# Optimization experiments

Measured on AMD Instinct MI355X. Metric: run time of the kernel, lower is better.

The kernel has to match this reference:

```python
import jax, jax.numpy as jnp
import numpy as np

N, NFEAT = 8192, 128

def _unif(k, shape, fan_out):
    s = 1.0 / np.sqrt(fan_out)
    return jax.random.uniform(k, shape, jnp.float32, -s, s)

def setup_inputs() -> dict:
    key = jax.random.key(0)
    ks = jax.random.split(key, 10)
    x = jax.random.normal(ks[0], (N, NFEAT), jnp.float32)
    adj = jax.random.uniform(ks[1], (N, N), jnp.float32)  # all > 0 -> full degree
    W1 = _unif(ks[2], (NFEAT, 10), 10); b1 = _unif(ks[3], (10,), 10)
    W2 = _unif(ks[4], (10, 5), 5);      b2 = _unif(ks[5], (5,), 5)
    fc1_W = _unif(ks[6], (5, 5), 5);    fc1_b = _unif(ks[7], (5,), 5)
    fc_W = _unif(ks[8], (5, 2), 2);     fc_b = _unif(ks[9], (2,), 2)
    return dict(x=x, adj=adj, W1=W1, b1=b1, W2=W2, b2=b2,
                fc1_W=fc1_W, fc1_b=fc1_b, fc_W=fc_W, fc_b=fc_b)

def _gcn(x, adj, W, b):
    # D = diag(row-wise count of adj > 0); A_tilda = D^-1/2 (A + I) D^-1/2
    deg = jnp.sum((adj > 0.0).astype(x.dtype), axis=1)
    dinv = deg ** -0.5                       # [N]
    s = (x @ W) * dinv[:, None]              # D^-1/2 @ (X W), [N, out]
    out = dinv[:, None] * (adj @ s + s)      # D^-1/2 @ (A + I) @ s
    return out + b

def reference(x, adj, W1, b1, W2, b2, fc1_W, fc1_b, fc_W, fc_b):
    h = jax.nn.relu(_gcn(x, adj, W1, b1))    # [N, 10]
    h = _gcn(h, adj, W2, b2)                 # [N, 5]
    z = jax.nn.relu(jnp.mean(h, axis=0))     # [5]
    z2 = jax.nn.relu(z @ fc1_W + fc1_b)      # [5]
    y = jax.nn.sigmoid(z2 @ fc_W + fc_b)     # [2]
    return (z, y)
```

## Files before the change

kernel.cpp:

```cpp
#include <hip/hip_runtime.h>
#include <math.h>

#define NN 8192
#define NF 128


__global__ __launch_bounds__(256) void kS1p(const float* __restrict__ x,
                                            const float* __restrict__ W1,
                                            float* __restrict__ s1p) {
    __shared__ float sW[NF * 10];
    for (int i = threadIdx.x; i < NF * 10; i += 256) sW[i] = W1[i];
    __syncthreads();
    int tid = blockIdx.x * 256 + threadIdx.x;
    int j = tid / 10, k = tid % 10;
    const float4* xr = (const float4*)(x + (size_t)j * NF);
    float s = 0.f;
#pragma unroll
    for (int f4 = 0; f4 < 32; f4++) {
        float4 a = xr[f4];
        s += a.x * sW[(f4 * 4 + 0) * 10 + k] + a.y * sW[(f4 * 4 + 1) * 10 + k]
           + a.z * sW[(f4 * 4 + 2) * 10 + k] + a.w * sW[(f4 * 4 + 3) * 10 + k];
    }
    s1p[tid] = s;
}

__global__ __launch_bounds__(512) void kFuse(const float* __restrict__ adj,
                                             const float* __restrict__ s1p,
                                             float* __restrict__ accO,
                                             float* __restrict__ dinv,
                                             float* __restrict__ c0,
                                             int* __restrict__ Zcount,
                                             int* __restrict__ Zlist) {
    __shared__ float lcs[4][2048];
    const int t = threadIdx.x;
    const int lane = t & 63, wid = t >> 6;
    for (int n = t; n < 8192; n += 512) ((float*)lcs)[n] = 0.f;
    __syncthreads();

    const int i0 = blockIdx.x * 32 + wid * 4;
    float acc[4][10];
#pragma unroll
    for (int r = 0; r < 4; r++)
#pragma unroll
        for (int k = 0; k < 10; k++) acc[r][k] = 0.f;
    int cnt[4] = {0, 0, 0, 0};

    const float4* a0p = (const float4*)(adj + (size_t)(i0 + 0) * NN);
    const float4* a1p = (const float4*)(adj + (size_t)(i0 + 1) * NN);
    const float4* a2p = (const float4*)(adj + (size_t)(i0 + 2) * NN);
    const float4* a3p = (const float4*)(adj + (size_t)(i0 + 3) * NN);

    for (int it = 0; it < 32; it++) {
        const int vi = it * 64 + lane;
        float4 a0 = a0p[vi], a1 = a1p[vi], a2 = a2p[vi], a3 = a3p[vi];
        const float4* sp = (const float4*)(s1p + (size_t)vi * 40);
        float sv[40];
#pragma unroll
        for (int q = 0; q < 10; q++) {
            float4 v = sp[q];
            sv[q * 4 + 0] = v.x; sv[q * 4 + 1] = v.y;
            sv[q * 4 + 2] = v.z; sv[q * 4 + 3] = v.w;
        }
#pragma unroll
        for (int k = 0; k < 10; k++) {
            acc[0][k] += a0.x * sv[k] + a0.y * sv[10 + k] + a0.z * sv[20 + k] + a0.w * sv[30 + k];
            acc[1][k] += a1.x * sv[k] + a1.y * sv[10 + k] + a1.z * sv[20 + k] + a1.w * sv[30 + k];
            acc[2][k] += a2.x * sv[k] + a2.y * sv[10 + k] + a2.z * sv[20 + k] + a2.w * sv[30 + k];
            acc[3][k] += a3.x * sv[k] + a3.y * sv[10 + k] + a3.z * sv[20 + k] + a3.w * sv[30 + k];
        }
        atomicAdd(&lcs[0][vi], a0.x + a1.x + a2.x + a3.x);
        atomicAdd(&lcs[1][vi], a0.y + a1.y + a2.y + a3.y);
        atomicAdd(&lcs[2][vi], a0.z + a1.z + a2.z + a3.z);
        atomicAdd(&lcs[3][vi], a0.w + a1.w + a2.w + a3.w);
        cnt[0] += (a0.x > 0.f) + (a0.y > 0.f) + (a0.z > 0.f) + (a0.w > 0.f);
        cnt[1] += (a1.x > 0.f) + (a1.y > 0.f) + (a1.z > 0.f) + (a1.w > 0.f);
        cnt[2] += (a2.x > 0.f) + (a2.y > 0.f) + (a2.z > 0.f) + (a2.w > 0.f);
        cnt[3] += (a3.x > 0.f) + (a3.y > 0.f) + (a3.z > 0.f) + (a3.w > 0.f);
    }

#pragma unroll
    for (int r = 0; r < 4; r++) {
#pragma unroll
        for (int k = 0; k < 10; k++)
#pragma unroll
            for (int off = 32; off > 0; off >>= 1)
                acc[r][k] += __shfl_xor(acc[r][k], off, 64);
#pragma unroll
        for (int off = 32; off > 0; off >>= 1)
            cnt[r] += __shfl_xor(cnt[r], off, 64);
    }

    if (lane == 0) {
#pragma unroll
        for (int r = 0; r < 4; r++) {
            const int i = i0 + r;
            dinv[i] = rsqrtf((float)cnt[r]);
            if (cnt[r] != NN) { int p = atomicAdd(Zcount, 1); Zlist[p] = i; }
#pragma unroll
            for (int k = 0; k < 10; k++) accO[i * 10 + k] = acc[r][k];
        }
    }

    __syncthreads();
    for (int n = t; n < 8192; n += 512)
        atomicAdd(&c0[n], lcs[n & 3][n >> 2]);
}

__global__ __launch_bounds__(256) void kTail(const float* __restrict__ adj,
                                             const float* __restrict__ accI,
                                             const float* __restrict__ s1p,
                                             const float* __restrict__ dinv,
                                             const float* __restrict__ c0,
                                             const int* __restrict__ Zcount,
                                             const int* __restrict__ Zlist,
                                             const float* __restrict__ b1,
                                             const float* __restrict__ W2,
                                             float* __restrict__ accum) {
    const int j = blockIdx.x * 256 + threadIdx.x;
    const float dinv0 = rsqrtf((float)NN);
    const float dj = dinv[j];
    float cj = c0[j] * dinv0;
    float hv[10];
#pragma unroll
    for (int k = 0; k < 10; k++) hv[k] = dinv0 * accI[j * 10 + k];

    const int zc = *Zcount;
    for (int p = 0; p < zc; p++) {
        const int zi = Zlist[p];
        const float dz = dinv[zi] - dinv0;
        cj += dz * adj[(size_t)zi * NN + j];
        const float az = dz * adj[(size_t)j * NN + zi];
#pragma unroll
        for (int k = 0; k < 10; k++) hv[k] += az * s1p[zi * 10 + k];
    }
#pragma unroll
    for (int k = 0; k < 10; k++)
        hv[k] = fmaxf(dj * (hv[k] + dj * s1p[j * 10 + k]) + b1[k], 0.f);

    float p10[10];
#pragma unroll
    for (int k = 0; k < 5; k++) {
        float s = 0.f;
#pragma unroll
        for (int m = 0; m < 10; m++) s += hv[m] * W2[m * 5 + k];
        s *= dj;
        p10[k] = cj * s;
        p10[5 + k] = dj * s;
    }
#pragma unroll
    for (int q = 0; q < 10; q++) {
        float v = p10[q];
#pragma unroll
        for (int off = 32; off > 0; off >>= 1) v += __shfl_xor(v, off, 64);
        if ((threadIdx.x & 63) == 0) atomicAdd(&accum[q], v);
    }
}

__global__ void kF2(const float* __restrict__ accum, const float* __restrict__ b2,
                    const float* __restrict__ fc1W, const float* __restrict__ fc1b,
                    const float* __restrict__ fcW, const float* __restrict__ fcb,
                    float* __restrict__ out) {
    if (threadIdx.x == 0 && blockIdx.x == 0) {
        float z[5];
        for (int k = 0; k < 5; k++) {
            float v = (accum[k] + accum[5 + k]) * (1.f / (float)NN) + b2[k];
            z[k] = fmaxf(v, 0.f);
            out[k] = z[k];
        }
        float z2[5];
        for (int m = 0; m < 5; m++) {
            float v = fc1b[m];
            for (int k = 0; k < 5; k++) v += z[k] * fc1W[k * 5 + m];
            z2[m] = fmaxf(v, 0.f);
        }
        for (int n = 0; n < 2; n++) {
            float v = fcb[n];
            for (int m = 0; m < 5; m++) v += z2[m] * fcW[m * 2 + n];
            out[5 + n] = 1.f / (1.f + expf(-v));
        }
    }
}

extern "C" void kernel_launch(void* const* d_in, const int* in_sizes, int n_in,
                              void* d_out, int out_size, void* d_ws, size_t ws_size,
                              hipStream_t stream) {
    const float* x    = (const float*)d_in[0];
    const float* adj  = (const float*)d_in[1];
    const float* W1   = (const float*)d_in[2];
    const float* b1   = (const float*)d_in[3];
    const float* W2   = (const float*)d_in[4];
    const float* b2   = (const float*)d_in[5];
    const float* fc1W = (const float*)d_in[6];
    const float* fc1b = (const float*)d_in[7];
    const float* fcW  = (const float*)d_in[8];
    const float* fcb  = (const float*)d_in[9];
    (void)in_sizes; (void)n_in; (void)out_size; (void)ws_size;

    float* ws    = (float*)d_ws;
    float* dinv  = ws;
    float* c0    = ws + 8192;
    float* s1p   = ws + 16384;
    float* acc   = ws + 98304;
    float* accum = ws + 180224;
    int*   Zcount = (int*)(ws + 180240);
    int*   Zlist  = (int*)(ws + 180244);
    float* out = (float*)d_out;

    hipMemsetAsync(c0, 0, 8192 * sizeof(float), stream);
    hipMemsetAsync(accum, 0, 20 * sizeof(float), stream);

    kS1p <<<320, 256, 0, stream>>>(x, W1, s1p);
    kFuse<<<256, 512, 0, stream>>>(adj, s1p, acc, dinv, c0, Zcount, Zlist);
    kTail<<<32,  256, 0, stream>>>(adj, acc, s1p, dinv, c0, Zcount, Zlist, b1, W2, accum);
    kF2  <<<1,   64,  0, stream>>>(accum, b2, fc1W, fc1b, fcW, fcb, out);
}
```

Before: 466.0 us.

## Double-buffer adjacency loads in kFuse and move degree counting to a sparse kernel

```diff
diff --git a/kernel.cpp b/kernel.cpp
--- a/kernel.cpp
+++ b/kernel.cpp
@@ -4,6 +4,10 @@
 #define NN 8192
 #define NF 128
 
+
+__device__ __forceinline__ float comp4(const float4& v, int c) {
+    return c == 0 ? v.x : c == 1 ? v.y : c == 2 ? v.z : v.w;
+}
 
 __global__ __launch_bounds__(256) void kS1p(const float* __restrict__ x,
                                             const float* __restrict__ W1,
@@ -43,59 +47,76 @@
     for (int r = 0; r < 4; r++)
 #pragma unroll
         for (int k = 0; k < 10; k++) acc[r][k] = 0.f;
-    int cnt[4] = {0, 0, 0, 0};
+    float rmin[4] = {1e30f, 1e30f, 1e30f, 1e30f};
 
     const float4* a0p = (const float4*)(adj + (size_t)(i0 + 0) * NN);
     const float4* a1p = (const float4*)(adj + (size_t)(i0 + 1) * NN);
     const float4* a2p = (const float4*)(adj + (size_t)(i0 + 2) * NN);
     const float4* a3p = (const float4*)(adj + (size_t)(i0 + 3) * NN);
-
-    for (int it = 0; it < 32; it++) {
-        const int vi = it * 64 + lane;
-        float4 a0 = a0p[vi], a1 = a1p[vi], a2 = a2p[vi], a3 = a3p[vi];
-        const float4* sp = (const float4*)(s1p + (size_t)vi * 40);
-        float sv[40];
-#pragma unroll
-        for (int q = 0; q < 10; q++) {
-            float4 v = sp[q];
-            sv[q * 4 + 0] = v.x; sv[q * 4 + 1] = v.y;
-            sv[q * 4 + 2] = v.z; sv[q * 4 + 3] = v.w;
-        }
-#pragma unroll
-        for (int k = 0; k < 10; k++) {
-            acc[0][k] += a0.x * sv[k] + a0.y * sv[10 + k] + a0.z * sv[20 + k] + a0.w * sv[30 + k];
-            acc[1][k] += a1.x * sv[k] + a1.y * sv[10 + k] + a1.z * sv[20 + k] + a1.w * sv[30 + k];
-            acc[2][k] += a2.x * sv[k] + a2.y * sv[10 + k] + a2.z * sv[20 + k] + a2.w * sv[30 + k];
-            acc[3][k] += a3.x * sv[k] + a3.y * sv[10 + k] + a3.z * sv[20 + k] + a3.w * sv[30 + k];
-        }
-        atomicAdd(&lcs[0][vi], a0.x + a1.x + a2.x + a3.x);
-        atomicAdd(&lcs[1][vi], a0.y + a1.y + a2.y + a3.y);
-        atomicAdd(&lcs[2][vi], a0.z + a1.z + a2.z + a3.z);
-        atomicAdd(&lcs[3][vi], a0.w + a1.w + a2.w + a3.w);
-        cnt[0] += (a0.x > 0.f) + (a0.y > 0.f) + (a0.z > 0.f) + (a0.w > 0.f);
-        cnt[1] += (a1.x > 0.f) + (a1.y > 0.f) + (a1.z > 0.f) + (a1.w > 0.f);
-        cnt[2] += (a2.x > 0.f) + (a2.y > 0.f) + (a2.z > 0.f) + (a2.w > 0.f);
-        cnt[3] += (a3.x > 0.f) + (a3.y > 0.f) + (a3.z > 0.f) + (a3.w > 0.f);
-    }
-
-#pragma unroll
-    for (int r = 0; r < 4; r++) {
+    const float4* spB = (const float4*)s1p;
+
+    auto loadT = [&](float4 (&A)[4], float4 (&S)[10], int v) {
+        A[0] = a0p[v]; A[1] = a1p[v]; A[2] = a2p[v]; A[3] = a3p[v];
+#pragma unroll
+        for (int q = 0; q < 10; q++) S[q] = spB[(size_t)v * 10 + q];
+    };
+
+    auto computeT = [&](const float4 (&A)[4], const float4 (&S)[10], int v) {
+        atomicAdd(&lcs[0][v], A[0].x + A[1].x + A[2].x + A[3].x);
+        atomicAdd(&lcs[1][v], A[0].y + A[1].y + A[2].y + A[3].y);
+        atomicAdd(&lcs[2][v], A[0].z + A[1].z + A[2].z + A[3].z);
+        atomicAdd(&lcs[3][v], A[0].w + A[1].w + A[2].w + A[3].w);
+#pragma unroll
+        for (int r = 0; r < 4; r++)
+            rmin[r] = fminf(rmin[r], fminf(fminf(A[r].x, A[r].y), fminf(A[r].z, A[r].w)));
+#pragma unroll
+        for (int jj = 0; jj < 4; jj++) {
+            const float a0c = comp4(A[0], jj), a1c = comp4(A[1], jj);
+            const float a2c = comp4(A[2], jj), a3c = comp4(A[3], jj);
+#pragma unroll
+            for (int k = 0; k < 10; k++) {
+                const int idx = jj * 10 + k;
+                const float s = comp4(S[idx >> 2], idx & 3);
+                acc[0][k] = fmaf(a0c, s, acc[0][k]);
+                acc[1][k] = fmaf(a1c, s, acc[1][k]);
+                acc[2][k] = fmaf(a2c, s, acc[2][k]);
+                acc[3][k] = fmaf(a3c, s, acc[3][k]);
+            }
+        }
+    };
+
+    float4 Aa[4], Ba[4];
+    float4 As[10], Bs[10];
+    int vi = lane;
+    loadT(Aa, As, vi);
+#pragma unroll 1
+    for (int it = 0; it < 15; it++) {
+        loadT(Ba, Bs, vi + 64);
+        computeT(Aa, As, vi);
+        loadT(Aa, As, vi + 128);
+        computeT(Ba, Bs, vi + 64);
+        vi += 128;
+    }
+    loadT(Ba, Bs, vi + 64);
+    computeT(Aa, As, vi);
+    computeT(Ba, Bs, vi + 64);
+
+#pragma unroll
+    for (int r = 0; r < 4; r++)
 #pragma unroll
         for (int k = 0; k < 10; k++)
 #pragma unroll
             for (int off = 32; off > 0; off >>= 1)
                 acc[r][k] += __shfl_xor(acc[r][k], off, 64);
-#pragma unroll
-        for (int off = 32; off > 0; off >>= 1)
-            cnt[r] += __shfl_xor(cnt[r], off, 64);
-    }
-
-    if (lane == 0) {
-#pragma unroll
-        for (int r = 0; r < 4; r++) {
+
+    const float dinv0 = rsqrtf((float)NN);
+#pragma unroll
+    for (int r = 0; r < 4; r++) {
+        unsigned long long anyz = __ballot(rmin[r] <= 0.f);
+        if (lane == 0) {
             const int i = i0 + r;
-            dinv[i] = rsqrtf((float)cnt[r]);
-            if (cnt[r] != NN) { int p = atomicAdd(Zcount, 1); Zlist[p] = i; }
+            dinv[i] = dinv0;
+            if (anyz) { int p = atomicAdd(Zcount, 1); Zlist[p] = i; }
 #pragma unroll
             for (int k = 0; k < 10; k++) accO[i * 10 + k] = acc[r][k];
         }
@@ -104,6 +125,31 @@
     __syncthreads();
     for (int n = t; n < 8192; n += 512)
         atomicAdd(&c0[n], lcs[n & 3][n >> 2]);
+}
+
+__global__ __launch_bounds__(256) void kZdeg(const float* __restrict__ adj,
+                                             const int* __restrict__ Zcount,
+                                             const int* __restrict__ Zlist,
+                                             float* __restrict__ dinv) {
+    __shared__ int wsum[4];
+    const int lane = threadIdx.x & 63, wid = threadIdx.x >> 6;
+    const int zc = *Zcount;
+    for (int p = blockIdx.x; p < zc; p += gridDim.x) {
+        const int zi = Zlist[p];
+        const float4* ar = (const float4*)(adj + (size_t)zi * NN);
+        int cnt = 0;
+        for (int v = threadIdx.x; v < 2048; v += 256) {
+            float4 a = ar[v];
+            cnt += (a.x > 0.f) + (a.y > 0.f) + (a.z > 0.f) + (a.w > 0.f);
+        }
+#pragma unroll
+        for (int off = 32; off > 0; off >>= 1) cnt += __shfl_xor(cnt, off, 64);
+        if (lane == 0) wsum[wid] = cnt;
+        __syncthreads();
+        if (threadIdx.x == 0)
+            dinv[zi] = rsqrtf((float)(wsum[0] + wsum[1] + wsum[2] + wsum[3]));
+        __syncthreads();
+    }
 }
 
 __global__ __launch_bounds__(256) void kTail(const float* __restrict__ adj,
@@ -199,18 +245,18 @@
     float* ws    = (float*)d_ws;
     float* dinv  = ws;
     float* c0    = ws + 8192;
-    float* s1p   = ws + 16384;
-    float* acc   = ws + 98304;
-    float* accum = ws + 180224;
-    int*   Zcount = (int*)(ws + 180240);
-    int*   Zlist  = (int*)(ws + 180244);
+    float* accum = ws + 16384;
+    int*   Zcount = (int*)(ws + 16394);
+    float* s1p   = ws + 16416;
+    float* acc   = ws + 98336;
+    int*   Zlist  = (int*)(ws + 180256);
     float* out = (float*)d_out;
 
-    hipMemsetAsync(c0, 0, 8192 * sizeof(float), stream);
-    hipMemsetAsync(accum, 0, 20 * sizeof(float), stream);
+    hipMemsetAsync(c0, 0, (8192 + 32) * sizeof(float), stream);
 
     kS1p <<<320, 256, 0, stream>>>(x, W1, s1p);
     kFuse<<<256, 512, 0, stream>>>(adj, s1p, acc, dinv, c0, Zcount, Zlist);
+    kZdeg<<<16,  256, 0, stream>>>(adj, Zcount, Zlist, dinv);
     kTail<<<32,  256, 0, stream>>>(adj, acc, s1p, dinv, c0, Zcount, Zlist, b1, W2, accum);
     kF2  <<<1,   64,  0, stream>>>(accum, b2, fc1W, fc1b, fcW, fcb, out);
 }
```

Result: faster. 446.3 us (-4.2%).
